# Kernel tuning notes

Hardware: AMD Instinct MI355X
Metric: run time of the kernel (lower is better)

## Reference

```python
import jax, jax.numpy as jnp
import numpy as np

B, S, DIN, DQ, DK = 8, 2048, 1024, 64, 64

def setup_inputs() -> dict:
    key = jax.random.key(0)
    ks = jax.random.split(key, 8)
    sc = 0.02
    return {
        "input_tensor": jax.random.normal(ks[0], (B, S, DIN), jnp.float32),
        "attention_mask": jax.random.randint(ks[1], (B, 1, S), 0, 2) == 1,
        "Wq": jax.random.normal(ks[2], (DIN, DQ), jnp.float32) * sc,
        "bq": jnp.zeros((DQ,), jnp.float32),
        "Wk": jax.random.normal(ks[3], (DIN, DK), jnp.float32) * sc,
        "bk": jnp.zeros((DK,), jnp.float32),
        "Wv": jax.random.normal(ks[4], (DIN, DK), jnp.float32) * sc,
        "bv": jnp.zeros((DK,), jnp.float32),
    }

def reference(input_tensor, attention_mask, Wq, bq, Wk, bk, Wv, bv):
    q = input_tensor @ Wq + bq          # [B,S,DQ]
    k = input_tensor @ Wk + bk          # [B,S,DK]
    v = input_tensor @ Wv + bv          # [B,S,DK]
    # NOTE: original scales by sqrt(query.size(1)) == sqrt(seq_len), faithfully kept
    scale = q.shape[1] ** 0.5
    scores = jnp.einsum('bqd,bkd->bqk', q, k) / scale
    scores = jnp.where(attention_mask, jnp.float32(-1e9), scores)
    attn = jax.nn.softmax(scores, axis=-1)
    context = jnp.einsum('bqk,bkd->bqd', attn, v)
    return context
```

## Files before the change

kernel.cpp:

```cpp
#include <hip/hip_runtime.h>
#include <hip/hip_bf16.h>

#define NB 8
#define SEQ 2048
#define DIN 1024
#define DH 64

typedef __attribute__((ext_vector_type(8))) short bf16x8;
typedef __attribute__((ext_vector_type(4))) float f32x4;
typedef __attribute__((ext_vector_type(4))) unsigned int u32x4;

static __device__ __forceinline__ unsigned short f2bf(float f) {
    unsigned int u = __builtin_bit_cast(unsigned int, f);
    unsigned int r = (u + 0x7FFFu + ((u >> 16) & 1u)) >> 16;
    return (unsigned short)r;
}

static __device__ __forceinline__ unsigned int cvt_pk_bf16(float lo, float hi) {
    unsigned int d;
    asm volatile("v_cvt_pk_bf16_f32 %0, %1, %2" : "=v"(d) : "v"(lo), "v"(hi));
    return d;
}

static __device__ __forceinline__ void gll16(const void* g, void* l) {
    __builtin_amdgcn_global_load_lds((const __attribute__((address_space(1))) unsigned int*)g,
                                     (__attribute__((address_space(3))) unsigned int*)l, 16, 0, 0);
}

#define WAITVM(N) asm volatile("s_waitcnt vmcnt(" #N ")" ::: "memory")

__global__ __launch_bounds__(256) void prep_kernel(
    const float* __restrict__ Wq, const float* __restrict__ Wk, const float* __restrict__ Wv,
    unsigned short* __restrict__ W3T)
{
    int j = blockIdx.x * 256 + threadIdx.x;
    int mat = j >> 16;
    int rem = j & 65535;
    int k = rem >> 6;
    int c = rem & 63;
    const float* W = (mat == 0) ? Wq : ((mat == 1) ? Wk : Wv);
    float v = W[rem];
    W3T[(size_t)(mat * 64 + c) * 1024 + k] = f2bf(v);
}

__global__ __launch_bounds__(256) void qkv_kernel(
    const float* __restrict__ X, const unsigned short* __restrict__ W3T,
    const float* __restrict__ bq, const float* __restrict__ bk, const float* __restrict__ bv,
    unsigned short* __restrict__ Qb, unsigned short* __restrict__ Kb, unsigned short* __restrict__ Vt)
{
    __shared__ __align__(16) unsigned char Xa[2][32768];
    __shared__ __align__(16) unsigned char Wt[2][8192];

    const int tid = threadIdx.x;
    const int w   = tid >> 6;
    const int l15 = tid & 15;
    const int lq  = (tid >> 4) & 3;
    const int wm  = w >> 1;
    const int wn  = w & 1;

    int bid = blockIdx.x;
    int sw = (bid & 7) * 48 + (bid >> 3);
    const int rt = sw / 3;
    const int ct = sw % 3;

    const char* Xgb = (const char*)(X + (size_t)rt * 128 * DIN);
    const char* Wgb = (const char*)W3T + (size_t)ct * 64 * 2048;

    int xr[8], xsrc[8];
    #pragma unroll
    for (int i = 0; i < 8; ++i) {
        int b = (i * 256 + tid) * 16;
        int r = b >> 8;
        int G = (b >> 5) & 7;
        int h = (b >> 4) & 1;
        xr[i] = b;
        xsrc[i] = r * 4096 + ((G ^ (r & 7)) << 5) + (h << 4);
    }
    int wr[2], wsrc[2];
    #pragma unroll
    for (int i = 0; i < 2; ++i) {
        int b = (i * 256 + tid) * 16;
        int col = b >> 7;
        int G = (b >> 4) & 7;
        wr[i] = b;
        wsrc[i] = col * 2048 + ((G ^ (col & 7)) << 4);
    }

    f32x4 acc[4][2] = {};

    #pragma unroll
    for (int i = 0; i < 8; ++i) gll16(Xgb + (size_t)xsrc[i], &Xa[0][xr[i]]);
    #pragma unroll
    for (int i = 0; i < 2; ++i) gll16(Wgb + (size_t)wsrc[i], &Wt[0][wr[i]]);

    #pragma unroll
    for (int t = 0; t < 16; ++t) {
        WAITVM(0);
        __builtin_amdgcn_s_barrier();
        __builtin_amdgcn_sched_barrier(0);

        if (t + 1 < 16) {
            #pragma unroll
            for (int i = 0; i < 8; ++i)
                gll16(Xgb + (size_t)xsrc[i] + (t + 1) * 256, &Xa[(t + 1) & 1][xr[i]]);
            #pragma unroll
            for (int i = 0; i < 2; ++i)
                gll16(Wgb + (size_t)wsrc[i] + (t + 1) * 128, &Wt[(t + 1) & 1][wr[i]]);
        }

        const unsigned char* xb = Xa[t & 1];
        const unsigned char* wb = Wt[t & 1];

        bf16x8 a[4][2];
        #pragma unroll
        for (int m = 0; m < 4; ++m) {
            int r = wm * 64 + m * 16 + l15;
            const unsigned char* rp = xb + r * 256;
            #pragma unroll
            for (int kk = 0; kk < 2; ++kk) {
                int g = (kk * 4 + lq) ^ (r & 7);
                f32x4 f0 = *(const f32x4*)(rp + g * 32);
                f32x4 f1 = *(const f32x4*)(rp + g * 32 + 16);
                u32x4 pk;
                pk[0] = cvt_pk_bf16(f0[0], f0[1]);
                pk[1] = cvt_pk_bf16(f0[2], f0[3]);
                pk[2] = cvt_pk_bf16(f1[0], f1[1]);
                pk[3] = cvt_pk_bf16(f1[2], f1[3]);
                a[m][kk] = __builtin_bit_cast(bf16x8, pk);
            }
        }
        bf16x8 bf[2][2];
        #pragma unroll
        for (int n = 0; n < 2; ++n) {
            int col = wn * 32 + n * 16 + l15;
            #pragma unroll
            for (int kk = 0; kk < 2; ++kk)
                bf[n][kk] = *(const bf16x8*)(wb + col * 128 + (((kk * 4 + lq) ^ (col & 7)) << 4));
        }
        #pragma unroll
        for (int kk = 0; kk < 2; ++kk)
            #pragma unroll
            for (int m = 0; m < 4; ++m)
                #pragma unroll
                for (int n = 0; n < 2; ++n)
                    acc[m][n] = __builtin_amdgcn_mfma_f32_16x16x32_bf16(a[m][kk], bf[n][kk], acc[m][n], 0, 0, 0);
    }

    const float* bvec = (ct == 0) ? bq : ((ct == 1) ? bk : bv);
    #pragma unroll
    for (int n = 0; n < 2; ++n) {
        int c = wn * 32 + n * 16 + l15;
        float badd = bvec[c];
        #pragma unroll
        for (int m = 0; m < 4; ++m) {
            #pragma unroll
            for (int reg = 0; reg < 4; ++reg) {
                int row = rt * 128 + wm * 64 + m * 16 + lq * 4 + reg;
                unsigned short v16 = f2bf(acc[m][n][reg] + badd);
                if (ct == 0)      Qb[(size_t)row * DH + c] = v16;
                else if (ct == 1) Kb[(size_t)row * DH + c] = v16;
                else {
                    int bb = row >> 11, ss = row & 2047;
                    Vt[((size_t)(bb * DH + c)) * SEQ + ss] = v16;
                }
            }
        }
    }
}

#define AKT 64
#define ANT 8
#define PP 36

__global__ __launch_bounds__(256) void attn_kernel(
    const unsigned short* __restrict__ Qb, const unsigned short* __restrict__ Kb,
    const unsigned short* __restrict__ Vt, const int* __restrict__ mask,
    float* __restrict__ Opart, float* __restrict__ lpart)
{
    __shared__ __align__(16) unsigned char Ksm[3][8192];
    __shared__ __align__(16) unsigned char Vsm[3][8192];
    __shared__ short ps[4][32][PP];
    __shared__ float sml[4][32];

    const int tid = threadIdx.x;
    const int w   = tid >> 6;
    const int l15 = tid & 15;
    const int lq  = (tid >> 4) & 3;
    const int wm  = w >> 1;
    const int wn  = w & 1;

    int bid = blockIdx.x;
    int sbid = (bid & 7) * 128 + (bid >> 3);
    const int b   = sbid >> 7;
    const int qt  = (sbid >> 2) & 31;
    const int kq  = sbid & 3;
    const int q0  = qt * 64;
    const int kb0 = kq * 512;

    bf16x8 aq[2][2];
    #pragma unroll
    for (int m = 0; m < 2; ++m)
        #pragma unroll
        for (int kk = 0; kk < 2; ++kk)
            aq[m][kk] = *(const bf16x8*)(Qb + ((size_t)(b * SEQ + q0 + wm * 32 + m * 16 + l15)) * DH + kk * 32 + lq * 8);

    int mk[ANT][2];
    #pragma unroll
    for (int t = 0; t < ANT; ++t) {
        mk[t][0] = mask[b * SEQ + kb0 + t * AKT + wn * 32 + l15];
        mk[t][1] = mask[b * SEQ + kb0 + t * AKT + wn * 32 + 16 + l15];
    }
    WAITVM(0);

    const char* Kg = (const char*)Kb + (size_t)(b * SEQ + kb0) * DH * 2;
    const char* Vg = (const char*)Vt + ((size_t)(b * DH) * SEQ + kb0) * 2;

    int slds[2], ksrc[2], vsrc[2];
    #pragma unroll
    for (int i = 0; i < 2; ++i) {
        int bb = i * 4096 + tid * 16;
        int row = bb >> 7;
        int g = (bb >> 4) & 7;
        int gs = g ^ (row & 7);
        slds[i] = bb;
        ksrc[i] = row * 128 + gs * 16;
        vsrc[i] = row * 4096 + gs * 16;
    }

    f32x4 o[2][4];
    #pragma unroll
    for (int m = 0; m < 2; ++m)
        #pragma unroll
        for (int n = 0; n < 4; ++n) o[m][n] = f32x4{0, 0, 0, 0};
    float lr[2][4] = {};
    const float rscale = 0.022097086912079612f;

    #pragma unroll
    for (int i = 0; i < 2; ++i) gll16(Kg + (size_t)ksrc[i], &Ksm[0][slds[i]]);
    #pragma unroll
    for (int i = 0; i < 2; ++i) gll16(Vg + (size_t)vsrc[i], &Vsm[0][slds[i]]);
    #pragma unroll
    for (int i = 0; i < 2; ++i) gll16(Kg + (size_t)8192 + ksrc[i], &Ksm[1][slds[i]]);
    #pragma unroll
    for (int i = 0; i < 2; ++i) gll16(Vg + (size_t)128 + vsrc[i], &Vsm[1][slds[i]]);

    #pragma unroll
    for (int t = 0; t < ANT; ++t) {
        if (t < ANT - 1) { WAITVM(4); } else { WAITVM(0); }
        __builtin_amdgcn_s_barrier();
        __builtin_amdgcn_sched_barrier(0);

        if (t + 2 < ANT) {
            int bi = (t + 2) % 3;
            #pragma unroll
            for (int i = 0; i < 2; ++i) gll16(Kg + (size_t)(t + 2) * 8192 + ksrc[i], &Ksm[bi][slds[i]]);
            #pragma unroll
            for (int i = 0; i < 2; ++i) gll16(Vg + (size_t)(t + 2) * 128 + vsrc[i], &Vsm[bi][slds[i]]);
        }

        const unsigned char* kt  = Ksm[t % 3];
        const unsigned char* vt2 = Vsm[t % 3];

        bf16x8 bkf[2][2];
        #pragma unroll
        for (int n = 0; n < 2; ++n)
            #pragma unroll
            for (int kk = 0; kk < 2; ++kk) {
                int row = wn * 32 + n * 16 + l15;
                bkf[n][kk] = *(const bf16x8*)(kt + row * 128 + ((4 * kk + lq) ^ (row & 7)) * 16);
            }
        f32x4 s[2][2];
        #pragma unroll
        for (int m = 0; m < 2; ++m)
            #pragma unroll
            for (int n = 0; n < 2; ++n) s[m][n] = f32x4{0, 0, 0, 0};
        #pragma unroll
        for (int kk = 0; kk < 2; ++kk)
            #pragma unroll
            for (int m = 0; m < 2; ++m)
                #pragma unroll
                for (int n = 0; n < 2; ++n)
                    s[m][n] = __builtin_amdgcn_mfma_f32_16x16x32_bf16(aq[m][kk], bkf[n][kk], s[m][n], 0, 0, 0);

        float bb0 = mk[t][0] ? -1e30f : 0.0f;
        float bb1 = mk[t][1] ? -1e30f : 0.0f;
        #pragma unroll
        for (int m = 0; m < 2; ++m)
            #pragma unroll
            for (int n = 0; n < 2; ++n) {
                float bvv = n ? bb1 : bb0;
                #pragma unroll
                for (int r = 0; r < 4; ++r) {
                    float p = __expf(fmaf(s[m][n][r], rscale, bvv));
                    lr[m][r] += p;
                    ps[w][m * 16 + lq * 4 + r][n * 16 + l15] = (short)f2bf(p);
                }
            }

        bf16x8 pa[2];
        #pragma unroll
        for (int m = 0; m < 2; ++m)
            pa[m] = *(const bf16x8*)&ps[w][m * 16 + l15][lq * 8];
        bf16x8 bvf[4];
        #pragma unroll
        for (int n = 0; n < 4; ++n) {
            int row = n * 16 + l15;
            bvf[n] = *(const bf16x8*)(vt2 + row * 128 + ((4 * wn + lq) ^ (row & 7)) * 16);
        }
        #pragma unroll
        for (int m = 0; m < 2; ++m)
            #pragma unroll
            for (int n = 0; n < 4; ++n)
                o[m][n] = __builtin_amdgcn_mfma_f32_16x16x32_bf16(pa[m], bvf[n], o[m][n], 0, 0, 0);
    }

    #pragma unroll
    for (int off = 1; off < 16; off <<= 1)
        #pragma unroll
        for (int m = 0; m < 2; ++m)
            #pragma unroll
            for (int r = 0; r < 4; ++r) lr[m][r] += __shfl_xor(lr[m][r], off);
    if (l15 == 0) {
        #pragma unroll
        for (int m = 0; m < 2; ++m)
            #pragma unroll
            for (int r = 0; r < 4; ++r) sml[w][m * 16 + lq * 4 + r] = lr[m][r];
    }
    __syncthreads();

    float (*mg)[32][64] = reinterpret_cast<float (*)[32][64]>(&Ksm[0][0]);
    if (wn == 1) {
        #pragma unroll
        for (int m = 0; m < 2; ++m)
            #pragma unroll
            for (int n = 0; n < 4; ++n)
                #pragma unroll
                for (int r = 0; r < 4; ++r)
                    mg[wm][m * 16 + lq * 4 + r][n * 16 + l15] = o[m][n][r];
    }
    __syncthreads();
    if (wn == 0) {
        #pragma unroll
        for (int m = 0; m < 2; ++m)
            #pragma unroll
            for (int n = 0; n < 4; ++n)
                #pragma unroll
                for (int r = 0; r < 4; ++r)
                    mg[wm][m * 16 + lq * 4 + r][n * 16 + l15] += o[m][n][r];
    }
    __syncthreads();

    {
        int qq = tid >> 2;
        int d0 = (tid & 3) * 16;
        float* dst = Opart + ((size_t)kq * (NB * SEQ) + b * SEQ + q0 + qq) * DH + d0;
        #pragma unroll
        for (int j = 0; j < 4; ++j)
            *(float4*)(dst + j * 4) = *(float4*)&mg[qq >> 5][qq & 31][d0 + j * 4];
    }
    if (tid < 64) {
        int wmi = tid >> 5;
        float lsum = sml[wmi * 2][tid & 31] + sml[wmi * 2 + 1][tid & 31];
        lpart[(size_t)kq * (NB * SEQ) + b * SEQ + q0 + tid] = lsum;
    }
}

__global__ __launch_bounds__(256) void merge_kernel(
    const float* __restrict__ Opart, const float* __restrict__ lpart,
    float* __restrict__ out)
{
    int bid = blockIdx.x;
    int sbid = (bid & 7) * 32 + (bid >> 3);
    int g = sbid * 256 + threadIdx.x;
    int q  = g >> 2;
    int d0 = (g & 3) * 16;

    float l = lpart[q] + lpart[16384 + q] + lpart[2 * 16384 + q] + lpart[3 * 16384 + q];
    float inv = 1.0f / l;

    const float* o0 = Opart + (size_t)q * DH + d0;
    #pragma unroll
    for (int j = 0; j < 4; ++j) {
        float4 a = *(const float4*)(o0 + j * 4);
        float4 b2 = *(const float4*)(o0 + (size_t)16384 * DH + j * 4);
        float4 c = *(const float4*)(o0 + (size_t)2 * 16384 * DH + j * 4);
        float4 d = *(const float4*)(o0 + (size_t)3 * 16384 * DH + j * 4);
        float4 r;
        r.x = (a.x + b2.x + c.x + d.x) * inv;
        r.y = (a.y + b2.y + c.y + d.y) * inv;
        r.z = (a.z + b2.z + c.z + d.z) * inv;
        r.w = (a.w + b2.w + c.w + d.w) * inv;
        *(float4*)(out + (size_t)q * DH + d0 + j * 4) = r;
    }
}

extern "C" void kernel_launch(void* const* d_in, const int* in_sizes, int n_in,
                              void* d_out, int out_size, void* d_ws, size_t ws_size,
                              hipStream_t stream) {
    const float* X    = (const float*)d_in[0];
    const int*   mask = (const int*)d_in[1];
    const float* Wq   = (const float*)d_in[2];
    const float* bq   = (const float*)d_in[3];
    const float* Wk   = (const float*)d_in[4];
    const float* bk   = (const float*)d_in[5];
    const float* Wv   = (const float*)d_in[6];
    const float* bv   = (const float*)d_in[7];
    float* out = (float*)d_out;

    char* ws = (char*)d_ws;
    unsigned short* Qb    = (unsigned short*)(ws);
    unsigned short* Kb    = (unsigned short*)(ws + (2u << 20));
    unsigned short* Vt    = (unsigned short*)(ws + (4u << 20));
    unsigned short* W3T   = (unsigned short*)(ws + (6u << 20));
    float* Opart          = (float*)(ws + (8u << 20));
    float* lpart          = (float*)(ws + (24u << 20));

    prep_kernel<<<768, 256, 0, stream>>>(Wq, Wk, Wv, W3T);
    qkv_kernel<<<384, 256, 0, stream>>>(X, W3T, bq, bk, bv, Qb, Kb, Vt);
    attn_kernel<<<1024, 256, 0, stream>>>(Qb, Kb, Vt, mask, Opart, lpart);
    merge_kernel<<<256, 256, 0, stream>>>(Opart, lpart, out);
}
```

Measured before the change: 67.35 us.

## Fuse QKV column tiles per block and widen attention blocks to 512 threads

The QKV projection now has each block cover 64 rows against all 192 output columns, so X is read from global memory once instead of three times, and the loads use a 3-stage pipeline with prefetch distance 2. The attention kernel moves to 512-thread blocks covering 128 queries, so each K/V tile staged in LDS is shared by twice as many waves, and each thread issues one load per tile. This cuts X and K/V traffic but gives fewer, larger blocks (256 and 512) and more LDS per block, which may lower occupancy.

```diff
diff --git a/kernel.cpp b/kernel.cpp
--- a/kernel.cpp
+++ b/kernel.cpp
@@ -48,27 +48,21 @@
     const float* __restrict__ bq, const float* __restrict__ bk, const float* __restrict__ bv,
     unsigned short* __restrict__ Qb, unsigned short* __restrict__ Kb, unsigned short* __restrict__ Vt)
 {
-    __shared__ __align__(16) unsigned char Xa[2][32768];
-    __shared__ __align__(16) unsigned char Wt[2][8192];
+    __shared__ __align__(16) unsigned char Xa[3][16384];
+    __shared__ __align__(16) unsigned char Wt[3][24576];
 
     const int tid = threadIdx.x;
     const int w   = tid >> 6;
     const int l15 = tid & 15;
     const int lq  = (tid >> 4) & 3;
-    const int wm  = w >> 1;
-    const int wn  = w & 1;
-
-    int bid = blockIdx.x;
-    int sw = (bid & 7) * 48 + (bid >> 3);
-    const int rt = sw / 3;
-    const int ct = sw % 3;
-
-    const char* Xgb = (const char*)(X + (size_t)rt * 128 * DIN);
-    const char* Wgb = (const char*)W3T + (size_t)ct * 64 * 2048;
-
-    int xr[8], xsrc[8];
-    #pragma unroll
-    for (int i = 0; i < 8; ++i) {
+    const int rt  = blockIdx.x;
+
+    const char* Xgb = (const char*)(X + (size_t)rt * 64 * DIN);
+    const char* Wgb = (const char*)W3T;
+
+    int xr[4], xsrc[4];
+    #pragma unroll
+    for (int i = 0; i < 4; ++i) {
         int b = (i * 256 + tid) * 16;
         int r = b >> 8;
         int G = (b >> 5) & 7;
@@ -76,45 +70,48 @@
         xr[i] = b;
         xsrc[i] = r * 4096 + ((G ^ (r & 7)) << 5) + (h << 4);
     }
-    int wr[2], wsrc[2];
-    #pragma unroll
-    for (int i = 0; i < 2; ++i) {
+    int wr6[6], wsrc6[6];
+    #pragma unroll
+    for (int i = 0; i < 6; ++i) {
         int b = (i * 256 + tid) * 16;
         int col = b >> 7;
-        int G = (b >> 4) & 7;
-        wr[i] = b;
-        wsrc[i] = col * 2048 + ((G ^ (col & 7)) << 4);
-    }
-
-    f32x4 acc[4][2] = {};
-
-    #pragma unroll
-    for (int i = 0; i < 8; ++i) gll16(Xgb + (size_t)xsrc[i], &Xa[0][xr[i]]);
-    #pragma unroll
-    for (int i = 0; i < 2; ++i) gll16(Wgb + (size_t)wsrc[i], &Wt[0][wr[i]]);
+        int g = (b >> 4) & 7;
+        wr6[i] = b;
+        wsrc6[i] = col * 2048 + ((g ^ (col & 7)) << 4);
+    }
+
+    f32x4 acc[4][3] = {};
+
+    #pragma unroll
+    for (int tt = 0; tt < 2; ++tt) {
+        #pragma unroll
+        for (int i = 0; i < 4; ++i) gll16(Xgb + (size_t)xsrc[i] + tt * 256, &Xa[tt][xr[i]]);
+        #pragma unroll
+        for (int i = 0; i < 6; ++i) gll16(Wgb + (size_t)wsrc6[i] + tt * 128, &Wt[tt][wr6[i]]);
+    }
 
     #pragma unroll
     for (int t = 0; t < 16; ++t) {
-        WAITVM(0);
+        if (t < 15) { WAITVM(10); } else { WAITVM(0); }
         __builtin_amdgcn_s_barrier();
         __builtin_amdgcn_sched_barrier(0);
 
-        if (t + 1 < 16) {
-            #pragma unroll
-            for (int i = 0; i < 8; ++i)
-                gll16(Xgb + (size_t)xsrc[i] + (t + 1) * 256, &Xa[(t + 1) & 1][xr[i]]);
-            #pragma unroll
-            for (int i = 0; i < 2; ++i)
-                gll16(Wgb + (size_t)wsrc[i] + (t + 1) * 128, &Wt[(t + 1) & 1][wr[i]]);
-        }
-
-        const unsigned char* xb = Xa[t & 1];
-        const unsigned char* wb = Wt[t & 1];
+        if (t + 2 < 16) {
+            int bi = (t + 2) % 3;
+            #pragma unroll
+            for (int i = 0; i < 4; ++i) gll16(Xgb + (size_t)xsrc[i] + (t + 2) * 256, &Xa[bi][xr[i]]);
+            #pragma unroll
+            for (int i = 0; i < 6; ++i) gll16(Wgb + (size_t)wsrc6[i] + (t + 2) * 128, &Wt[bi][wr6[i]]);
+        }
+        __builtin_amdgcn_sched_barrier(0);
+
+        const unsigned char* xb = Xa[t % 3];
+        const unsigned char* wb = Wt[t % 3];
 
         bf16x8 a[4][2];
         #pragma unroll
         for (int m = 0; m < 4; ++m) {
-            int r = wm * 64 + m * 16 + l15;
+            int r = m * 16 + l15;
             const unsigned char* rp = xb + r * 256;
             #pragma unroll
             for (int kk = 0; kk < 2; ++kk) {
@@ -129,10 +126,10 @@
                 a[m][kk] = __builtin_bit_cast(bf16x8, pk);
             }
         }
-        bf16x8 bf[2][2];
-        #pragma unroll
-        for (int n = 0; n < 2; ++n) {
-            int col = wn * 32 + n * 16 + l15;
+        bf16x8 bf[3][2];
+        #pragma unroll
+        for (int n = 0; n < 3; ++n) {
+            int col = w * 48 + n * 16 + l15;
             #pragma unroll
             for (int kk = 0; kk < 2; ++kk)
                 bf[n][kk] = *(const bf16x8*)(wb + col * 128 + (((kk * 4 + lq) ^ (col & 7)) << 4));
@@ -142,23 +139,23 @@
             #pragma unroll
             for (int m = 0; m < 4; ++m)
                 #pragma unroll
-                for (int n = 0; n < 2; ++n)
+                for (int n = 0; n < 3; ++n)
                     acc[m][n] = __builtin_amdgcn_mfma_f32_16x16x32_bf16(a[m][kk], bf[n][kk], acc[m][n], 0, 0, 0);
     }
 
-    const float* bvec = (ct == 0) ? bq : ((ct == 1) ? bk : bv);
-    #pragma unroll
-    for (int n = 0; n < 2; ++n) {
-        int c = wn * 32 + n * 16 + l15;
-        float badd = bvec[c];
+    #pragma unroll
+    for (int n = 0; n < 3; ++n) {
+        int col = w * 48 + n * 16 + l15;
+        int mat = col >> 6, c = col & 63;
+        float badd = ((mat == 0) ? bq : ((mat == 1) ? bk : bv))[c];
         #pragma unroll
         for (int m = 0; m < 4; ++m) {
             #pragma unroll
             for (int reg = 0; reg < 4; ++reg) {
-                int row = rt * 128 + wm * 64 + m * 16 + lq * 4 + reg;
+                int row = rt * 64 + m * 16 + lq * 4 + reg;
                 unsigned short v16 = f2bf(acc[m][n][reg] + badd);
-                if (ct == 0)      Qb[(size_t)row * DH + c] = v16;
-                else if (ct == 1) Kb[(size_t)row * DH + c] = v16;
+                if (mat == 0)      Qb[(size_t)row * DH + c] = v16;
+                else if (mat == 1) Kb[(size_t)row * DH + c] = v16;
                 else {
                     int bb = row >> 11, ss = row & 2047;
                     Vt[((size_t)(bb * DH + c)) * SEQ + ss] = v16;
@@ -172,29 +169,29 @@
 #define ANT 8
 #define PP 36
 
-__global__ __launch_bounds__(256) void attn_kernel(
+__global__ __launch_bounds__(512) void attn_kernel(
     const unsigned short* __restrict__ Qb, const unsigned short* __restrict__ Kb,
     const unsigned short* __restrict__ Vt, const int* __restrict__ mask,
     float* __restrict__ Opart, float* __restrict__ lpart)
 {
     __shared__ __align__(16) unsigned char Ksm[3][8192];
     __shared__ __align__(16) unsigned char Vsm[3][8192];
-    __shared__ short ps[4][32][PP];
-    __shared__ float sml[4][32];
+    __shared__ short ps[8][32][PP];
+    __shared__ float sml[8][32];
 
     const int tid = threadIdx.x;
     const int w   = tid >> 6;
     const int l15 = tid & 15;
     const int lq  = (tid >> 4) & 3;
-    const int wm  = w >> 1;
+    const int wq  = w >> 1;
     const int wn  = w & 1;
 
     int bid = blockIdx.x;
-    int sbid = (bid & 7) * 128 + (bid >> 3);
-    const int b   = sbid >> 7;
-    const int qt  = (sbid >> 2) & 31;
+    int sbid = (bid & 7) * 64 + (bid >> 3);
+    const int b   = sbid >> 6;
+    const int qt  = (sbid >> 2) & 15;
     const int kq  = sbid & 3;
-    const int q0  = qt * 64;
+    const int q0  = qt * 128;
     const int kb0 = kq * 512;
 
     bf16x8 aq[2][2];
@@ -202,7 +199,7 @@
     for (int m = 0; m < 2; ++m)
         #pragma unroll
         for (int kk = 0; kk < 2; ++kk)
-            aq[m][kk] = *(const bf16x8*)(Qb + ((size_t)(b * SEQ + q0 + wm * 32 + m * 16 + l15)) * DH + kk * 32 + lq * 8);
+            aq[m][kk] = *(const bf16x8*)(Qb + ((size_t)(b * SEQ + q0 + wq * 32 + m * 16 + l15)) * DH + kk * 32 + lq * 8);
 
     int mk[ANT][2];
     #pragma unroll
@@ -215,17 +212,12 @@
     const char* Kg = (const char*)Kb + (size_t)(b * SEQ + kb0) * DH * 2;
     const char* Vg = (const char*)Vt + ((size_t)(b * DH) * SEQ + kb0) * 2;
 
-    int slds[2], ksrc[2], vsrc[2];
-    #pragma unroll
-    for (int i = 0; i < 2; ++i) {
-        int bb = i * 4096 + tid * 16;
-        int row = bb >> 7;
-        int g = (bb >> 4) & 7;
-        int gs = g ^ (row & 7);
-        slds[i] = bb;
-        ksrc[i] = row * 128 + gs * 16;
-        vsrc[i] = row * 4096 + gs * 16;
-    }
+    const int srow = tid >> 3;
+    const int scolb = (tid & 7) * 16;
+    const int sldsb = tid * 16;
+    const int gsw = ((scolb >> 4) ^ (srow & 7)) << 4;
+    const int ksrc = srow * 128 + gsw;
+    const int vsrc = srow * 4096 + gsw;
 
     f32x4 o[2][4];
     #pragma unroll
@@ -236,27 +228,23 @@
     const float rscale = 0.022097086912079612f;
 
     #pragma unroll
-    for (int i = 0; i < 2; ++i) gll16(Kg + (size_t)ksrc[i], &Ksm[0][slds[i]]);
-    #pragma unroll
-    for (int i = 0; i < 2; ++i) gll16(Vg + (size_t)vsrc[i], &Vsm[0][slds[i]]);
-    #pragma unroll
-    for (int i = 0; i < 2; ++i) gll16(Kg + (size_t)8192 + ksrc[i], &Ksm[1][slds[i]]);
-    #pragma unroll
-    for (int i = 0; i < 2; ++i) gll16(Vg + (size_t)128 + vsrc[i], &Vsm[1][slds[i]]);
+    for (int tt = 0; tt < 2; ++tt) {
+        gll16(Kg + (size_t)ksrc + tt * 8192, &Ksm[tt][sldsb]);
+        gll16(Vg + (size_t)vsrc + tt * 128,  &Vsm[tt][sldsb]);
+    }
 
     #pragma unroll
     for (int t = 0; t < ANT; ++t) {
-        if (t < ANT - 1) { WAITVM(4); } else { WAITVM(0); }
+        if (t < ANT - 1) { WAITVM(2); } else { WAITVM(0); }
         __builtin_amdgcn_s_barrier();
         __builtin_amdgcn_sched_barrier(0);
 
         if (t + 2 < ANT) {
             int bi = (t + 2) % 3;
-            #pragma unroll
-            for (int i = 0; i < 2; ++i) gll16(Kg + (size_t)(t + 2) * 8192 + ksrc[i], &Ksm[bi][slds[i]]);
-            #pragma unroll
-            for (int i = 0; i < 2; ++i) gll16(Vg + (size_t)(t + 2) * 128 + vsrc[i], &Vsm[bi][slds[i]]);
-        }
+            gll16(Kg + (size_t)ksrc + (t + 2) * 8192, &Ksm[bi][sldsb]);
+            gll16(Vg + (size_t)vsrc + (t + 2) * 128,  &Vsm[bi][sldsb]);
+        }
+        __builtin_amdgcn_sched_barrier(0);
 
         const unsigned char* kt  = Ksm[t % 3];
         const unsigned char* vt2 = Vsm[t % 3];
@@ -336,7 +324,7 @@
             for (int n = 0; n < 4; ++n)
                 #pragma unroll
                 for (int r = 0; r < 4; ++r)
-                    mg[wm][m * 16 + lq * 4 + r][n * 16 + l15] = o[m][n][r];
+                    mg[wq][m * 16 + lq * 4 + r][n * 16 + l15] = o[m][n][r];
     }
     __syncthreads();
     if (wn == 0) {
@@ -346,7 +334,7 @@
             for (int n = 0; n < 4; ++n)
                 #pragma unroll
                 for (int r = 0; r < 4; ++r)
-                    mg[wm][m * 16 + lq * 4 + r][n * 16 + l15] += o[m][n][r];
+                    mg[wq][m * 16 + lq * 4 + r][n * 16 + l15] += o[m][n][r];
     }
     __syncthreads();
 
@@ -358,7 +346,7 @@
         for (int j = 0; j < 4; ++j)
             *(float4*)(dst + j * 4) = *(float4*)&mg[qq >> 5][qq & 31][d0 + j * 4];
     }
-    if (tid < 64) {
+    if (tid < 128) {
         int wmi = tid >> 5;
         float lsum = sml[wmi * 2][tid & 31] + sml[wmi * 2 + 1][tid & 31];
         lpart[(size_t)kq * (NB * SEQ) + b * SEQ + q0 + tid] = lsum;
@@ -416,7 +404,7 @@
     float* lpart          = (float*)(ws + (24u << 20));
 
     prep_kernel<<<768, 256, 0, stream>>>(Wq, Wk, Wv, W3T);
-    qkv_kernel<<<384, 256, 0, stream>>>(X, W3T, bq, bk, bv, Qb, Kb, Vt);
-    attn_kernel<<<1024, 256, 0, stream>>>(Qb, Kb, Vt, mask, Opart, lpart);
+    qkv_kernel<<<256, 256, 0, stream>>>(X, W3T, bq, bk, bv, Qb, Kb, Vt);
+    attn_kernel<<<512, 512, 0, stream>>>(Qb, Kb, Vt, mask, Opart, lpart);
     merge_kernel<<<256, 256, 0, stream>>>(Opart, lpart, out);
 }
```

New measurement: 69.47 us. +3.1%, slower.
